# Performance work log

Measured on AMD Instinct MI355X. Metric: run time of the kernel, lower is better.

## Reference

```python
import jax, jax.numpy as jnp
import numpy as np

VOCAB = 32000
EMB = 1024
BLOCK = 2048
B = 4


def setup_inputs() -> dict:
    key = jax.random.key(0)
    ks = jax.random.split(key, 10)
    s = EMB ** -0.5
    return {
        "idx": jax.random.randint(ks[0], (B, BLOCK), 0, VOCAB),
        "targets": jax.random.randint(ks[1], (B, BLOCK), 0, VOCAB),
        "tok_emb": jax.random.normal(ks[2], (VOCAB, EMB), jnp.float32),
        "pos_emb": jax.random.normal(ks[3], (BLOCK, EMB), jnp.float32),
        "Wk": jax.random.normal(ks[4], (EMB, EMB), jnp.float32) * s,
        "Wq": jax.random.normal(ks[5], (EMB, EMB), jnp.float32) * s,
        "Wv": jax.random.normal(ks[6], (EMB, EMB), jnp.float32) * s,
        "Wlm": jax.random.normal(ks[7], (EMB, VOCAB), jnp.float32) * s,
        "blm": jnp.zeros((VOCAB,), jnp.float32),
    }


def reference(idx, targets, tok_emb, pos_emb, Wk, Wq, Wv, Wlm, blm):
    B_, T = idx.shape
    x = tok_emb[idx] + pos_emb[:T]  # [B,T,C]
    C = x.shape[-1]
    k = x @ Wk  # [B,T,H]
    q = x @ Wq
    v = x @ Wv
    wei = jnp.einsum("bth,bsh->bts", q, k) * (C ** -0.5)  # [B,T,T]
    causal = jnp.tril(jnp.ones((T, T), bool))
    wei = jnp.where(causal, wei, -jnp.inf)
    wei = jax.nn.softmax(wei, axis=-1)
    out = jnp.einsum("bts,bsh->bth", wei, v)  # [B,T,H]
    logits = out @ Wlm + blm  # [B,T,V]
    logits2d = logits.reshape(B_ * T, -1)
    tgt = targets.reshape(B_ * T)
    logp = jax.nn.log_softmax(logits2d, axis=-1)
    loss = -jnp.mean(jnp.take_along_axis(logp, tgt[:, None], axis=1))
    return logits2d, loss
```

## Files before the change

### kernel.cpp

```cpp
#include <hip/hip_runtime.h>
#include <hip/hip_bf16.h>
#include <cstdint>

#define VOCAB 32000
#define EMB   1024
#define TLEN  2048
#define NB    4
#define MTOT  (NB*TLEN)

typedef __bf16 bf16;
typedef __bf16 bf16x8 __attribute__((ext_vector_type(8)));
typedef float  f32x4  __attribute__((ext_vector_type(4)));

__global__ __launch_bounds__(256)
void embed_wt_kernel(const int* __restrict__ idx,
                     const float* __restrict__ tok,
                     const float* __restrict__ pos,
                     bf16* __restrict__ x,
                     const float* __restrict__ Wq,
                     const float* __restrict__ Wk,
                     const float* __restrict__ Wv,
                     bf16* __restrict__ Wqk_t,
                     bf16* __restrict__ Wv_t)
{
    __shared__ bf16 tile[64][65];
    const int q = blockIdx.x, tid = threadIdx.x;
    if (q < 4096) {
        int gid = q * 256 + tid;
        int r   = gid >> 7;
        int c0  = (gid & 127) << 3;
        int t   = r & (TLEN - 1);
        int tk  = idx[r];
        const float4* tp = reinterpret_cast<const float4*>(tok + (long)tk * EMB + c0);
        const float4* pp = reinterpret_cast<const float4*>(pos + (long)t  * EMB + c0);
        float4 a0 = tp[0], a1 = tp[1];
        float4 b0 = pp[0], b1 = pp[1];
        bf16x8 o;
        o[0] = (bf16)(a0.x + b0.x); o[1] = (bf16)(a0.y + b0.y);
        o[2] = (bf16)(a0.z + b0.z); o[3] = (bf16)(a0.w + b0.w);
        o[4] = (bf16)(a1.x + b1.x); o[5] = (bf16)(a1.y + b1.y);
        o[6] = (bf16)(a1.z + b1.z); o[7] = (bf16)(a1.w + b1.w);
        *reinterpret_cast<bf16x8*>(x + (long)r * EMB + c0) = o;
    } else {
        const int q2  = q - 4096;
        const int sel = q2 >> 8;
        const int t   = q2 & 255;
        const float* W = (sel == 0) ? Wq : (sel == 1) ? Wk : Wv;
        bf16* Wt = (sel == 0) ? Wqk_t : (sel == 1) ? (Wqk_t + 1024 * 1024) : Wv_t;
        const int n0 = (t & 15) * 64;
        const int k0 = (t >> 4) * 64;
        int c  = tid & 63, r0 = tid >> 6;
#pragma unroll
        for (int i = 0; i < 16; ++i) {
            int r = r0 + i * 4;
            tile[r][c] = (bf16)W[(long)(k0 + r) * EMB + n0 + c];
        }
        __syncthreads();
        int kc = tid & 63, nr0 = tid >> 6;
#pragma unroll
        for (int i = 0; i < 16; ++i) {
            int nr = nr0 + i * 4;
            Wt[(long)(n0 + nr) * EMB + k0 + kc] = tile[kc][nr];
        }
    }
}

__device__ __forceinline__ void gll16(const void* g, void* l)
{
    __builtin_amdgcn_global_load_lds(
        (const __attribute__((address_space(1))) unsigned int*)g,
        (__attribute__((address_space(3))) unsigned int*)l, 16, 0, 0);
}

__device__ __forceinline__ void stage256s(const bf16* __restrict__ gbase,
                                          int ld, int kt, bf16* lbase, int tid)
{
#pragma unroll
    for (int p = 0; p < 4; ++p) {
        int lin  = p * 512 + tid;
        int row  = lin >> 3;
        int slot = lin & 7;
        int ke   = ((slot ^ (row & 7)) << 3) + kt;
        gll16(gbase + (long)row * ld + ke, lbase + lin * 8);
    }
}

template<int CMODE>
__device__ __forceinline__ void gemm256_body(
    const bf16* __restrict__ A, int lda, long sA,
    const bf16* __restrict__ Bt, int ldb, long sB,
    bf16* __restrict__ C, int ldc, long sC, int K,
    int bx, int by, int zb, bf16* smem, int tid)
{
    bf16* As = smem;
    bf16* Bs = smem + 32768;

    const int lane = tid & 63, wid = tid >> 6;
    const int wr = wid >> 2, wc = wid & 3;
    const int l15 = lane & 15, hi = lane >> 4, l7 = lane & 7;

    const bf16* Ab = A  + (long)zb * sA + (long)(by * 256) * lda;
    const bf16* Bb = Bt + (long)zb * sB + (long)(bx * 256) * ldb;

    const int Keff = (CMODE == 2) ? ((by + 1) * 256) : K;
    const int NT   = Keff >> 6;

    f32x4 acc[8][4] = {};

    stage256s(Ab, lda, 0, As, tid);
    stage256s(Bb, ldb, 0, Bs, tid);
    __syncthreads();

#pragma unroll 1
    for (int t = 0; t < NT; ++t) {
        const int buf = t & 1;
        if (t + 1 < NT) {
            stage256s(Ab, lda, (t + 1) * 64, As + (buf ^ 1) * 16384, tid);
            stage256s(Bb, ldb, (t + 1) * 64, Bs + (buf ^ 1) * 16384, tid);
        }
        const bf16* Ap = As + buf * 16384 + (wr * 128) * 64;
        const bf16* Bp = Bs + buf * 16384 + (wc * 64) * 64;
#pragma unroll
        for (int ks = 0; ks < 2; ++ks) {
            const int ko = 8 * (((ks << 2) | hi) ^ l7);
            bf16x8 bfr[4];
#pragma unroll
            for (int n = 0; n < 4; ++n)
                bfr[n] = *(const bf16x8*)(Bp + (n * 16 + l15) * 64 + ko);
#pragma unroll
            for (int m = 0; m < 8; ++m) {
                bf16x8 af = *(const bf16x8*)(Ap + (m * 16 + l15) * 64 + ko);
#pragma unroll
                for (int n = 0; n < 4; ++n)
                    acc[m][n] = __builtin_amdgcn_mfma_f32_16x16x32_bf16(
                                    af, bfr[n], acc[m][n], 0, 0, 0);
            }
        }
        __syncthreads();
    }

    bf16* Cb = C + (long)zb * sC;
    const int colb = bx * 256 + wc * 64 + l15;
    const int rowb = by * 256 + wr * 128 + (hi << 2);
#pragma unroll
    for (int m = 0; m < 8; ++m)
#pragma unroll
        for (int n = 0; n < 4; ++n)
#pragma unroll
            for (int r = 0; r < 4; ++r)
                Cb[(long)(rowb + m * 16 + r) * ldc + colb + n * 16] =
                    (bf16)acc[m][n][r];
}

template<int CMODE>
__global__ __launch_bounds__(512)
void gemm256_bt(const bf16* __restrict__ A, int lda, long sA,
                const bf16* __restrict__ Bt, int ldb, long sB,
                bf16* __restrict__ C, int ldc, long sC, int K)
{
    extern __shared__ bf16 smem[];
    gemm256_body<CMODE>(A, lda, sA, Bt, ldb, sB, C, ldc, sC, K,
                        blockIdx.x, blockIdx.y, blockIdx.z, smem, threadIdx.x);
}

__global__ __launch_bounds__(512)
void fused_vt_s(const bf16* __restrict__ Wv_t, const bf16* __restrict__ x,
                bf16* __restrict__ v_t,
                const bf16* __restrict__ qk, bf16* __restrict__ S)
{
    extern __shared__ bf16 smem[];
    const int q = blockIdx.x, tid = threadIdx.x;
    if (q < 128) {
        gemm256_body<0>(Wv_t, EMB, 0, x, EMB, 0, v_t, MTOT, 0, EMB,
                        q & 31, q >> 5, 0, smem, tid);
    } else {
        int q2 = q - 128;
        int z = q2 / 36, t = q2 % 36;
        int by = 0, a = 0;
        while (a + by + 1 <= t) { a += by + 1; ++by; }
        int bx = t - a;
        gemm256_body<0>(qk, 2048, (long)TLEN * 2048,
                        qk + 1024, 2048, (long)TLEN * 2048,
                        S, TLEN, (long)TLEN * TLEN, EMB, bx, by, z, smem, tid);
    }
}

__global__ __launch_bounds__(512)
void fused_pv_wt(const bf16* __restrict__ P, const bf16* __restrict__ v_t,
                 bf16* __restrict__ att,
                 const float* __restrict__ Wlm, bf16* __restrict__ Wlm_t)
{
    extern __shared__ bf16 smem[];
    const int q = blockIdx.x, tid = threadIdx.x;
    if (q < 128) {
        gemm256_body<2>(P, TLEN, (long)TLEN * TLEN, v_t, MTOT, (long)TLEN,
                        att, EMB, (long)TLEN * EMB, TLEN,
                        q & 3, (q >> 2) & 7, q >> 5, smem, tid);
    } else {
        const int q2 = q - 128;
        const int n0 = (q2 % 125) * 256;
        const int k0 = (q2 / 125) * 64;
        bf16 (*tile)[257] = (bf16(*)[257])smem;
#pragma unroll
        for (int i = 0; i < 8; ++i) {
            int lin = i * 512 + tid;
            int r = lin >> 6, c4 = lin & 63;
            float4 v = *(const float4*)(Wlm + (long)(k0 + r) * VOCAB + n0 + c4 * 4);
            tile[r][c4 * 4 + 0] = (bf16)v.x;
            tile[r][c4 * 4 + 1] = (bf16)v.y;
            tile[r][c4 * 4 + 2] = (bf16)v.z;
            tile[r][c4 * 4 + 3] = (bf16)v.w;
        }
        __syncthreads();
#pragma unroll
        for (int i = 0; i < 4; ++i) {
            int lin = i * 512 + tid;
            int nr = lin >> 3, kc8 = (lin & 7) * 8;
            bf16x8 o;
#pragma unroll
            for (int j = 0; j < 8; ++j) o[j] = tile[kc8 + j][nr];
            *(bf16x8*)(Wlm_t + (long)(n0 + nr) * EMB + k0 + kc8) = o;
        }
    }
}

__global__ __launch_bounds__(512)
void gemm256_logits(const bf16* __restrict__ A, const bf16* __restrict__ Bt,
                    float* __restrict__ C, const float* __restrict__ bias,
                    float2* __restrict__ part)
{
    extern __shared__ bf16 smem[];
    bf16* As = smem;
    bf16* Bs = smem + 32768;

    const int tid  = threadIdx.x;
    const int lane = tid & 63, wid = tid >> 6;
    const int wr = wid >> 2, wc = wid & 3;
    const int l15 = lane & 15, hi = lane >> 4, l7 = lane & 7;

    const int wg = blockIdx.x;
    const int xcd = wg & 7, c = wg >> 3;
    const int nb = c >> 2;
    const int mb = xcd * 4 + (c & 3);

    const bf16* Ab = A  + (long)(mb * 256) * EMB;
    const bf16* Bb = Bt + (long)(nb * 256) * EMB;

    const long colbase = (long)nb * 256 + wc * 64 + l15;
    float bv[4];
#pragma unroll
    for (int n = 0; n < 4; ++n) bv[n] = bias[colbase + n * 16];

    f32x4 acc[8][4] = {};

    stage256s(Ab, EMB, 0, As, tid);
    stage256s(Bb, EMB, 0, Bs, tid);
    __syncthreads();

    const int NT = EMB / 64;
#pragma unroll 1
    for (int t = 0; t < NT; ++t) {
        const int buf = t & 1;
        if (t + 1 < NT) {
            stage256s(Ab, EMB, (t + 1) * 64, As + (buf ^ 1) * 16384, tid);
            stage256s(Bb, EMB, (t + 1) * 64, Bs + (buf ^ 1) * 16384, tid);
        }
        const bf16* Ap = As + buf * 16384 + (wr * 128) * 64;
        const bf16* Bp = Bs + buf * 16384 + (wc * 64) * 64;
#pragma unroll
        for (int ks = 0; ks < 2; ++ks) {
            const int ko = 8 * (((ks << 2) | hi) ^ l7);
            bf16x8 bfr[4];
#pragma unroll
            for (int n = 0; n < 4; ++n)
                bfr[n] = *(const bf16x8*)(Bp + (n * 16 + l15) * 64 + ko);
#pragma unroll
            for (int m = 0; m < 8; ++m) {
                bf16x8 af = *(const bf16x8*)(Ap + (m * 16 + l15) * 64 + ko);
#pragma unroll
                for (int n = 0; n < 4; ++n)
                    acc[m][n] = __builtin_amdgcn_mfma_f32_16x16x32_bf16(
                                    af, bfr[n], acc[m][n], 0, 0, 0);
            }
        }
        __syncthreads();
    }

    float* pm = (float*)smem;
    float* ps = pm + 1024;

    const long rowbase = (long)mb * 256 + wr * 128;
#pragma unroll
    for (int m = 0; m < 8; ++m) {
#pragma unroll
        for (int r = 0; r < 4; ++r) {
            float v0 = acc[m][0][r] + bv[0];
            float v1 = acc[m][1][r] + bv[1];
            float v2 = acc[m][2][r] + bv[2];
            float v3 = acc[m][3][r] + bv[3];
            long row = rowbase + m * 16 + (hi << 2) + r;
            float* Cp = C + row * (long)VOCAB + colbase;
            __builtin_nontemporal_store(v0, Cp);
            __builtin_nontemporal_store(v1, Cp + 16);
            __builtin_nontemporal_store(v2, Cp + 32);
            __builtin_nontemporal_store(v3, Cp + 48);

            float lm = fmaxf(fmaxf(v0, v1), fmaxf(v2, v3));
#pragma unroll
            for (int o = 1; o < 16; o <<= 1) lm = fmaxf(lm, __shfl_xor(lm, o));
            float sp = __expf(v0 - lm) + __expf(v1 - lm) +
                       __expf(v2 - lm) + __expf(v3 - lm);
#pragma unroll
            for (int o = 1; o < 16; o <<= 1) sp += __shfl_xor(sp, o);
            if (l15 == 0) {
                int rb = wr * 128 + m * 16 + (hi << 2) + r;
                pm[wc * 256 + rb] = lm;
                ps[wc * 256 + rb] = sp;
            }
        }
    }
    __syncthreads();
    if (tid < 256) {
        float m0 = pm[tid], m1 = pm[256 + tid], m2 = pm[512 + tid], m3 = pm[768 + tid];
        float M = fmaxf(fmaxf(m0, m1), fmaxf(m2, m3));
        float S = ps[tid] * __expf(m0 - M) + ps[256 + tid] * __expf(m1 - M) +
                  ps[512 + tid] * __expf(m2 - M) + ps[768 + tid] * __expf(m3 - M);
        part[(long)nb * MTOT + mb * 256 + tid] = make_float2(M, S);
    }
}

__global__ void softmax_causal_kernel(const bf16* __restrict__ S,
                                      bf16* __restrict__ P)
{
    const int r = blockIdx.x;
    const int t = r & (TLEN - 1);
    const int limit = ((t >> 8) + 1) << 8;
    const int tid = threadIdx.x;
    const int lane = tid & 63, wv = tid >> 6;
    const float scale = 0.03125f;
    const int c0 = tid * 8;

    float v[8];
    float m = -1e30f;
    if (c0 < limit) {
        bf16x8 sv = *(const bf16x8*)(S + (long)r * TLEN + c0);
#pragma unroll
        for (int i = 0; i < 8; ++i) {
            float x = (c0 + i <= t) ? (float)sv[i] * scale : -1e30f;
            v[i] = x;
            m = fmaxf(m, x);
        }
    } else {
#pragma unroll
        for (int i = 0; i < 8; ++i) v[i] = -1e30f;
    }
    __shared__ float red[4];
#pragma unroll
    for (int off = 32; off; off >>= 1) m = fmaxf(m, __shfl_xor(m, off));
    if (lane == 0) red[wv] = m;
    __syncthreads();
    m = fmaxf(fmaxf(red[0], red[1]), fmaxf(red[2], red[3]));
    __syncthreads();

    float s = 0.f;
#pragma unroll
    for (int i = 0; i < 8; ++i) { v[i] = __expf(v[i] - m); s += v[i]; }
#pragma unroll
    for (int off = 32; off; off >>= 1) s += __shfl_xor(s, off);
    if (lane == 0) red[wv] = s;
    __syncthreads();
    s = red[0] + red[1] + red[2] + red[3];
    float inv = 1.0f / s;
    if (c0 < limit) {
        bf16x8 o;
#pragma unroll
        for (int i = 0; i < 8; ++i) o[i] = (bf16)(v[i] * inv);
        *(bf16x8*)(P + (long)r * TLEN + c0) = o;
    }
}

__global__ void loss_combine_kernel(const float2* __restrict__ part,
                                    const float* __restrict__ logits,
                                    const int* __restrict__ tgt,
                                    float* __restrict__ bsum)
{
    const int tid = threadIdx.x;
    const int row = blockIdx.x * 256 + tid;
    const int lane = tid & 63, wv = tid >> 6;
    float M = -1e30f, S = 0.f;
    for (int i = 0; i < 125; ++i) {
        float2 v = part[(long)i * MTOT + row];
        if (v.x <= M) S += v.y * __expf(v.x - M);
        else { S = S * __expf(M - v.x) + v.y; M = v.x; }
    }
    float lse = M + __logf(S);
    float l = lse - logits[(long)row * VOCAB + tgt[row]];
#pragma unroll
    for (int off = 32; off; off >>= 1) l += __shfl_xor(l, off);
    __shared__ float red[4];
    if (lane == 0) red[wv] = l;
    __syncthreads();
    if (tid == 0) bsum[blockIdx.x] = red[0] + red[1] + red[2] + red[3];
}

__global__ void loss_final_kernel(const float* __restrict__ bsum,
                                  float* __restrict__ out)
{
    const int lane = threadIdx.x;
    float s = (lane < 32) ? bsum[lane] : 0.f;
#pragma unroll
    for (int off = 32; off; off >>= 1) s += __shfl_xor(s, off);
    if (lane == 0) out[0] = s * (1.0f / MTOT);
}

extern "C" void kernel_launch(void* const* d_in, const int* in_sizes, int n_in,
                              void* d_out, int out_size, void* d_ws, size_t ws_size,
                              hipStream_t stream)
{
    const int*   idx = (const int*)  d_in[0];
    const int*   tgt = (const int*)  d_in[1];
    const float* tok = (const float*)d_in[2];
    const float* pos = (const float*)d_in[3];
    const float* Wk  = (const float*)d_in[4];
    const float* Wq  = (const float*)d_in[5];
    const float* Wv  = (const float*)d_in[6];
    const float* Wlm = (const float*)d_in[7];
    const float* blm = (const float*)d_in[8];
    float* out = (float*)d_out;

    char* ws = (char*)d_ws;
    if (ws_size < (size_t)140 * 1024 * 1024) return;

    bf16*   x     = (bf16*)(ws);
    bf16*   qk    = (bf16*)(ws + (16l << 20));
    bf16*   v_t   = (bf16*)(ws + (48l << 20));
    bf16*   S     = (bf16*)(ws + (64l << 20));
    bf16*   Wqk_t = (bf16*)(ws + (96l << 20));
    bf16*   Wv_t  = (bf16*)(ws + (100l << 20));
    bf16*   att   = (bf16*)(ws);
    bf16*   P     = (bf16*)(ws + (16l << 20));
    bf16*   Wlm_t = (bf16*)(ws + (64l << 20));
    float2* part  = (float2*)(ws + (127l << 20));
    float*  bsum  = (float*)(ws + (135l << 20));

    embed_wt_kernel<<<dim3(4864), 256, 0, stream>>>(
        idx, tok, pos, x, Wq, Wk, Wv, Wqk_t, Wv_t);

    gemm256_bt<0><<<dim3(2048 / 256, MTOT / 256, 1), 512, 131072, stream>>>(
        x, EMB, 0, Wqk_t, EMB, 0, qk, 2048, 0, EMB);

    fused_vt_s<<<dim3(272), 512, 131072, stream>>>(Wv_t, x, v_t, qk, S);

    softmax_causal_kernel<<<dim3(MTOT), 256, 0, stream>>>(S, P);

    fused_pv_wt<<<dim3(2128), 512, 131072, stream>>>(P, v_t, att, Wlm, Wlm_t);

    gemm256_logits<<<dim3(4000), 512, 131072, stream>>>(att, Wlm_t, out, blm, part);

    loss_combine_kernel<<<dim3(32), 256, 0, stream>>>(part, out, tgt, bsum);
    loss_final_kernel<<<dim3(1), 64, 0, stream>>>(bsum, out + (long)MTOT * VOCAB);
}
```

Baseline: 821.4 us.

## Retile logits GEMM to 256x128 blocks with small static LDS for occupancy

The logits GEMM moves from 256x256 tiles with 512 threads and 128KB dynamic LDS to 256x128 tiles with 256 threads, a K-step of 32 and about 48KB of static LDS with a new swizzle. More workgroups can then be resident per CU, which is meant to improve latency hiding and balance across the larger grid. In exchange, A-tile reuse per block halves, there are twice as many loop iterations and barriers, and the partial log-sum-exp buffer and combine loop double from 125 to 250 column blocks. The partial buffer is moved to reuse the freed P region of the workspace.

```diff
diff --git a/kernel.cpp b/kernel.cpp
--- a/kernel.cpp
+++ b/kernel.cpp
@@ -224,19 +224,36 @@
     }
 }
 
-__global__ __launch_bounds__(512)
+__device__ __forceinline__ void stageL(const bf16* __restrict__ g, int rows,
+                                       int kt, bf16* l, int tid)
+{
+    const int iters = rows >> 6;
+#pragma unroll
+    for (int p = 0; p < 4; ++p) {
+        if (p < iters) {
+            int lin  = p * 256 + tid;
+            int row  = lin >> 2;
+            int slot = lin & 3;
+            int ke   = ((slot ^ ((row >> 1) & 3)) << 3) + kt;
+            gll16(g + (long)row * EMB + ke, l + lin * 8);
+        }
+    }
+}
+
+__global__ __launch_bounds__(256)
 void gemm256_logits(const bf16* __restrict__ A, const bf16* __restrict__ Bt,
                     float* __restrict__ C, const float* __restrict__ bias,
                     float2* __restrict__ part)
 {
-    extern __shared__ bf16 smem[];
-    bf16* As = smem;
-    bf16* Bs = smem + 32768;
+    __shared__ bf16 As[2][256 * 32];
+    __shared__ bf16 Bs[2][128 * 32];
+    __shared__ float pm[2][256];
+    __shared__ float ps[2][256];
 
     const int tid  = threadIdx.x;
     const int lane = tid & 63, wid = tid >> 6;
-    const int wr = wid >> 2, wc = wid & 3;
-    const int l15 = lane & 15, hi = lane >> 4, l7 = lane & 7;
+    const int wr = wid >> 1, wc = wid & 1;
+    const int l15 = lane & 15, hi = lane >> 4;
 
     const int wg = blockIdx.x;
     const int xcd = wg & 7, c = wg >> 3;
@@ -244,50 +261,47 @@
     const int mb = xcd * 4 + (c & 3);
 
     const bf16* Ab = A  + (long)(mb * 256) * EMB;
-    const bf16* Bb = Bt + (long)(nb * 256) * EMB;
-
-    const long colbase = (long)nb * 256 + wc * 64 + l15;
+    const bf16* Bb = Bt + (long)(nb * 128) * EMB;
+
+    const long colbase = (long)nb * 128 + wc * 64 + l15;
     float bv[4];
 #pragma unroll
     for (int n = 0; n < 4; ++n) bv[n] = bias[colbase + n * 16];
 
     f32x4 acc[8][4] = {};
 
-    stage256s(Ab, EMB, 0, As, tid);
-    stage256s(Bb, EMB, 0, Bs, tid);
-    __syncthreads();
-
-    const int NT = EMB / 64;
+    const int ko = 8 * (hi ^ ((l15 >> 1) & 3));
+    const bf16* ApR = &As[0][0] + (wr * 128 + l15) * 32 + ko;
+    const bf16* BpR = &Bs[0][0] + (wc * 64  + l15) * 32 + ko;
+
+    stageL(Ab, 256, 0, &As[0][0], tid);
+    stageL(Bb, 128, 0, &Bs[0][0], tid);
+    __syncthreads();
+
+    const int NT = EMB / 32;
 #pragma unroll 1
     for (int t = 0; t < NT; ++t) {
         const int buf = t & 1;
         if (t + 1 < NT) {
-            stage256s(Ab, EMB, (t + 1) * 64, As + (buf ^ 1) * 16384, tid);
-            stage256s(Bb, EMB, (t + 1) * 64, Bs + (buf ^ 1) * 16384, tid);
-        }
-        const bf16* Ap = As + buf * 16384 + (wr * 128) * 64;
-        const bf16* Bp = Bs + buf * 16384 + (wc * 64) * 64;
-#pragma unroll
-        for (int ks = 0; ks < 2; ++ks) {
-            const int ko = 8 * (((ks << 2) | hi) ^ l7);
-            bf16x8 bfr[4];
+            stageL(Ab, 256, (t + 1) * 32, &As[buf ^ 1][0], tid);
+            stageL(Bb, 128, (t + 1) * 32, &Bs[buf ^ 1][0], tid);
+        }
+        const bf16* Ap = ApR + buf * (256 * 32);
+        const bf16* Bp = BpR + buf * (128 * 32);
+        bf16x8 bfr[4];
+#pragma unroll
+        for (int n = 0; n < 4; ++n)
+            bfr[n] = *(const bf16x8*)(Bp + (n * 16) * 32);
+#pragma unroll
+        for (int m = 0; m < 8; ++m) {
+            bf16x8 af = *(const bf16x8*)(Ap + (m * 16) * 32);
 #pragma unroll
             for (int n = 0; n < 4; ++n)
-                bfr[n] = *(const bf16x8*)(Bp + (n * 16 + l15) * 64 + ko);
-#pragma unroll
-            for (int m = 0; m < 8; ++m) {
-                bf16x8 af = *(const bf16x8*)(Ap + (m * 16 + l15) * 64 + ko);
-#pragma unroll
-                for (int n = 0; n < 4; ++n)
-                    acc[m][n] = __builtin_amdgcn_mfma_f32_16x16x32_bf16(
-                                    af, bfr[n], acc[m][n], 0, 0, 0);
-            }
+                acc[m][n] = __builtin_amdgcn_mfma_f32_16x16x32_bf16(
+                                af, bfr[n], acc[m][n], 0, 0, 0);
         }
         __syncthreads();
     }
-
-    float* pm = (float*)smem;
-    float* ps = pm + 1024;
 
     const long rowbase = (long)mb * 256 + wr * 128;
 #pragma unroll
@@ -314,17 +328,17 @@
             for (int o = 1; o < 16; o <<= 1) sp += __shfl_xor(sp, o);
             if (l15 == 0) {
                 int rb = wr * 128 + m * 16 + (hi << 2) + r;
-                pm[wc * 256 + rb] = lm;
-                ps[wc * 256 + rb] = sp;
+                pm[wc][rb] = lm;
+                ps[wc][rb] = sp;
             }
         }
     }
     __syncthreads();
-    if (tid < 256) {
-        float m0 = pm[tid], m1 = pm[256 + tid], m2 = pm[512 + tid], m3 = pm[768 + tid];
-        float M = fmaxf(fmaxf(m0, m1), fmaxf(m2, m3));
-        float S = ps[tid] * __expf(m0 - M) + ps[256 + tid] * __expf(m1 - M) +
-                  ps[512 + tid] * __expf(m2 - M) + ps[768 + tid] * __expf(m3 - M);
+    {
+        float m0 = pm[0][tid], m1 = pm[1][tid];
+        float s0 = ps[0][tid], s1 = ps[1][tid];
+        float M = fmaxf(m0, m1);
+        float S = s0 * __expf(m0 - M) + s1 * __expf(m1 - M);
         part[(long)nb * MTOT + mb * 256 + tid] = make_float2(M, S);
     }
 }
@@ -388,7 +402,7 @@
     const int row = blockIdx.x * 256 + tid;
     const int lane = tid & 63, wv = tid >> 6;
     float M = -1e30f, S = 0.f;
-    for (int i = 0; i < 125; ++i) {
+    for (int i = 0; i < 250; ++i) {
         float2 v = part[(long)i * MTOT + row];
         if (v.x <= M) S += v.y * __expf(v.x - M);
         else { S = S * __expf(M - v.x) + v.y; M = v.x; }
@@ -440,8 +454,8 @@
     bf16*   att   = (bf16*)(ws);
     bf16*   P     = (bf16*)(ws + (16l << 20));
     bf16*   Wlm_t = (bf16*)(ws + (64l << 20));
-    float2* part  = (float2*)(ws + (127l << 20));
-    float*  bsum  = (float*)(ws + (135l << 20));
+    float2* part  = (float2*)(ws + (16l << 20));
+    float*  bsum  = (float*)(ws + (33l << 20));
 
     embed_wt_kernel<<<dim3(4864), 256, 0, stream>>>(
         idx, tok, pos, x, Wq, Wk, Wv, Wqk_t, Wv_t);
@@ -455,7 +469,7 @@
 
     fused_pv_wt<<<dim3(2128), 512, 131072, stream>>>(P, v_t, att, Wlm, Wlm_t);
 
-    gemm256_logits<<<dim3(4000), 512, 131072, stream>>>(att, Wlm_t, out, blm, part);
+    gemm256_logits<<<dim3(8000), 256, 0, stream>>>(att, Wlm_t, out, blm, part);
 
     loss_combine_kernel<<<dim3(32), 256, 0, stream>>>(part, out, tgt, bsum);
     loss_final_kernel<<<dim3(1), 64, 0, stream>>>(bsum, out + (long)MTOT * VOCAB);
```

New measurement: 1.538 ms. 1.87x slower.
